# Kernel optimization log

Hardware: AMD Instinct MI355X
Metric: run time of the kernel (lower is better)

## Reference

```python
import jax, jax.numpy as jnp
import numpy as np

NUM_HEADS = 16


def setup_inputs() -> dict:
    key = jax.random.key(0)
    k1, k2, k3 = jax.random.split(key, 3)
    B, S, D = 4, 2048, 1024
    x = jax.random.normal(k1, (B, S, D), dtype=jnp.float32)
    w_qkv = jax.random.normal(k2, (D, 3 * D), dtype=jnp.float32) * 0.02
    b_qkv = jnp.zeros((3 * D,), dtype=jnp.float32)
    w_proj = jax.random.normal(k3, (D, D), dtype=jnp.float32) * 0.02
    b_proj = jnp.zeros((D,), dtype=jnp.float32)
    return {"x": x, "w_qkv": w_qkv, "b_qkv": b_qkv, "w_proj": w_proj, "b_proj": b_proj}


def reference(x, w_qkv, b_qkv, w_proj, b_proj):
    B, S, D = x.shape
    H = NUM_HEADS
    hd = D // H
    # fused qkv projection: [B,S,3D] -> [B,S,3H,hd]
    qkv = (x @ w_qkv + b_qkv).reshape(B, S, 3 * H, hd)
    q, k, v = jnp.split(qkv, 3, axis=2)  # each [B,S,H,hd]
    scale = (1.0 / jnp.sqrt(hd)).astype(x.dtype)
    scores = jnp.einsum("bqhd,bkhd->bhqk", q, k) * scale  # [B,H,S,S]
    causal = jnp.tril(jnp.ones((S, S), dtype=bool))  # [S,S]
    masked = jnp.where(causal, scores, jnp.finfo(scores.dtype).min)
    # softmax in fp32 reduce dtype, cast back (dropout_rate=0 -> identity)
    attn = jax.nn.softmax(masked.astype(jnp.float32)).astype(masked.dtype)
    out = jnp.einsum("bhqk,bkhd->bqhd", attn, v).reshape(B, S, D)
    return out @ w_proj + b_proj
```

## Files before the change

kernel.cpp:

```cpp
#include <hip/hip_runtime.h>
#include <hip/hip_bf16.h>

typedef __attribute__((ext_vector_type(8))) short short8;
typedef __attribute__((ext_vector_type(4))) float f32x4;

#define B_   4
#define S_   2048
#define D_   1024
#define H_   16
#define HD_  64
#define M_   (B_ * S_)
#define N3_  (3 * D_)

#define GLDS16(g, l)                                                        \
  __builtin_amdgcn_global_load_lds(                                         \
      (const __attribute__((address_space(1))) void*)(g),                   \
      (__attribute__((address_space(3))) void*)(l), 16, 0, 0)

template <int CTRL>
__device__ __forceinline__ float dpp_maxf(float x) {
  int v = __builtin_amdgcn_update_dpp(0, __builtin_bit_cast(int, x), CTRL,
                                      0xf, 0xf, true);
  return fmaxf(x, __builtin_bit_cast(float, v));
}
__device__ __forceinline__ float red16_max(float x) {
  x = dpp_maxf<0xB1>(x);
  x = dpp_maxf<0x4E>(x);
  x = dpp_maxf<0x141>(x);
  x = dpp_maxf<0x140>(x);
  return x;
}

__global__ __launch_bounds__(256) void cast_f32_bf16(
    const float* __restrict__ in, __hip_bfloat16* __restrict__ out, int n) {
  int i = (blockIdx.x * 256 + threadIdx.x) * 4;
  if (i + 3 < n) {
    float4 v = *(const float4*)(in + i);
    union { ushort4 u4; __hip_bfloat16 h[4]; } p;
    p.h[0] = __float2bfloat16(v.x);
    p.h[1] = __float2bfloat16(v.y);
    p.h[2] = __float2bfloat16(v.z);
    p.h[3] = __float2bfloat16(v.w);
    *(ushort4*)(out + i) = p.u4;
  }
}

__global__ __launch_bounds__(256) void transpose_cast(
    const float* __restrict__ in, __hip_bfloat16* __restrict__ out,
    int rows, int cols) {
  __shared__ float tile[32][33];
  int bx = blockIdx.x * 32;
  int by = blockIdx.y * 32;
  int tx = threadIdx.x, ty = threadIdx.y;
#pragma unroll
  for (int i = 0; i < 4; ++i)
    tile[ty + i * 8][tx] = in[(size_t)(by + ty + i * 8) * cols + bx + tx];
  __syncthreads();
#pragma unroll
  for (int i = 0; i < 4; ++i)
    out[(size_t)(bx + ty + i * 8) * rows + by + tx] =
        __float2bfloat16(tile[tx][ty + i * 8]);
}

__global__ __launch_bounds__(512) void transpose_v(
    const __hip_bfloat16* __restrict__ qkv, __hip_bfloat16* __restrict__ vt) {
  __shared__ __hip_bfloat16 tile[64][65];
  const int sb = blockIdx.x * 64;
  const int bh = blockIdx.y;
  const int b = bh >> 4, hh = bh & 15;
  const int tx = threadIdx.x, ty = threadIdx.y;
  const size_t src = (size_t)b * S_ * N3_ + 2 * D_ + hh * HD_;
#pragma unroll
  for (int i = 0; i < 8; ++i)
    tile[ty + i * 8][tx] = qkv[src + (size_t)(sb + ty + i * 8) * N3_ + tx];
  __syncthreads();
  const size_t dst = (size_t)bh * HD_ * S_;
#pragma unroll
  for (int i = 0; i < 8; ++i)
    vt[dst + (size_t)(ty + i * 8) * S_ + sb + tx] = tile[tx][ty + i * 8];
}

__device__ inline void store_out(float* p, float v) { *p = v; }
__device__ inline void store_out(__hip_bfloat16* p, float v) {
  *p = __float2bfloat16(v);
}

template <typename OUT_T>
__global__ __launch_bounds__(256) void gemm_bt_bias(
    const __hip_bfloat16* __restrict__ A, const __hip_bfloat16* __restrict__ Bt,
    const float* __restrict__ bias, OUT_T* __restrict__ C,
    int M, int N, int K) {
  __shared__ __align__(16) __hip_bfloat16 Alds[128 * 32];
  __shared__ __align__(16) __hip_bfloat16 Blds[128 * 32];
  const int t = threadIdx.x;
  const int wave = t >> 6, lane = t & 63;
  const int quad = lane >> 4, l15 = lane & 15;
  const int wm = (wave >> 1) * 64, wn = (wave & 1) * 64;
  const int m0 = blockIdx.y * 128, n0 = blockIdx.x * 128;

  const int rsub = lane >> 2;
  const int swz = (rsub ^ (rsub >> 2)) & 3;
  const int gcol = 8 * ((lane & 3) ^ swz);
  const int c0 = wave * 2, c1 = c0 + 1;
  const __hip_bfloat16* gA0 = A + (size_t)(m0 + c0 * 16 + rsub) * K + gcol;
  const __hip_bfloat16* gA1 = A + (size_t)(m0 + c1 * 16 + rsub) * K + gcol;
  const __hip_bfloat16* gB0 = Bt + (size_t)(n0 + c0 * 16 + rsub) * K + gcol;
  const __hip_bfloat16* gB1 = Bt + (size_t)(n0 + c1 * 16 + rsub) * K + gcol;
  __hip_bfloat16* lA0 = Alds + c0 * 512;
  __hip_bfloat16* lA1 = Alds + c1 * 512;
  __hip_bfloat16* lB0 = Blds + c0 * 512;
  __hip_bfloat16* lB1 = Blds + c1 * 512;
  const int swr = (l15 ^ (l15 >> 2)) & 3;
  const int fcol = 8 * (quad ^ swr);

  f32x4 acc[4][4] = {};

  for (int k0 = 0; k0 < K; k0 += 32) {
    GLDS16(gA0 + k0, lA0);
    GLDS16(gA1 + k0, lA1);
    GLDS16(gB0 + k0, lB0);
    GLDS16(gB1 + k0, lB1);
    __syncthreads();
    short8 a[4], bfr[4];
#pragma unroll
    for (int mt = 0; mt < 4; ++mt)
      a[mt] = *(const short8*)(Alds + (wm + mt * 16 + l15) * 32 + fcol);
#pragma unroll
    for (int nt = 0; nt < 4; ++nt)
      bfr[nt] = *(const short8*)(Blds + (wn + nt * 16 + l15) * 32 + fcol);
#pragma unroll
    for (int mt = 0; mt < 4; ++mt)
#pragma unroll
      for (int nt = 0; nt < 4; ++nt)
        acc[mt][nt] = __builtin_amdgcn_mfma_f32_16x16x32_bf16(
            a[mt], bfr[nt], acc[mt][nt], 0, 0, 0);
    __syncthreads();
  }

#pragma unroll
  for (int mt = 0; mt < 4; ++mt)
#pragma unroll
    for (int nt = 0; nt < 4; ++nt) {
      int col = n0 + wn + nt * 16 + l15;
      float bv = bias[col];
#pragma unroll
      for (int r = 0; r < 4; ++r) {
        int row = m0 + wm + mt * 16 + quad * 4 + r;
        store_out(C + (size_t)row * N + col, acc[mt][nt][r] + bv);
      }
    }
}

__global__ __launch_bounds__(256) void attn_causal(
    const __hip_bfloat16* __restrict__ qkv,
    const __hip_bfloat16* __restrict__ vt,
    __hip_bfloat16* __restrict__ ctx) {
  __shared__ __align__(16) __hip_bfloat16 Klds[64][72];
  __shared__ __align__(16) __hip_bfloat16 Vlds[64][72];
  __shared__ __align__(16) __hip_bfloat16 Plds[4][16][68];

  const int t = threadIdx.x;
  const int wave = t >> 6, lane = t & 63;
  const int quad = lane >> 4, l15 = lane & 15;
  const int xb = blockIdx.x, h = blockIdx.y, b = blockIdx.z;

  const size_t qbase = (size_t)b * S_ * N3_ + h * HD_;
  const size_t kbase = qbase + D_;
  const size_t vtbase = (size_t)(b * H_ + h) * HD_ * S_;
  const float C2 = 0.18033688f;

  short8 ones;
#pragma unroll
  for (int j = 0; j < 8; ++j) ones[j] = (short)0x3F80;

  for (int sel = 0; sel < 2; ++sel) {
    const int qb = sel ? (31 - xb) : xb;
    const int qrow = qb * 64 + wave * 16 + l15;
    short8 qf0 = *(const short8*)(qkv + qbase + (size_t)qrow * N3_ + quad * 8);
    short8 qf1 =
        *(const short8*)(qkv + qbase + (size_t)qrow * N3_ + 32 + quad * 8);

    f32x4 o[4] = {};
    float m_r[4], l_r[4];
#pragma unroll
    for (int r = 0; r < 4; ++r) { m_r[r] = -1e30f; l_r[r] = 0.f; }

    for (int kb = 0; kb <= qb; ++kb) {
#pragma unroll
      for (int i = 0; i < 2; ++i) {
        int c = t + 256 * i;
        int row = c >> 3, seg = c & 7;
        *(uint4*)(&Klds[row][seg * 8]) = *(const uint4*)(
            qkv + kbase + (size_t)(kb * 64 + row) * N3_ + seg * 8);
        *(uint4*)(&Vlds[row][seg * 8]) = *(const uint4*)(
            vt + vtbase + (size_t)row * S_ + kb * 64 + seg * 8);
      }
      __syncthreads();

      f32x4 s[4];
#pragma unroll
      for (int nt = 0; nt < 4; ++nt) {
        f32x4 z = {};
        short8 k0 = *(const short8*)(&Klds[nt * 16 + l15][quad * 8]);
        short8 k1 = *(const short8*)(&Klds[nt * 16 + l15][32 + quad * 8]);
        z = __builtin_amdgcn_mfma_f32_16x16x32_bf16(qf0, k0, z, 0, 0, 0);
        z = __builtin_amdgcn_mfma_f32_16x16x32_bf16(qf1, k1, z, 0, 0, 0);
        s[nt] = z;
      }
      const bool diag = (kb == qb);
#pragma unroll
      for (int nt = 0; nt < 4; ++nt)
#pragma unroll
        for (int r = 0; r < 4; ++r) {
          float v = s[nt][r] * C2;
          if (diag) {
            int colg = nt * 16 + l15;
            int rowg = wave * 16 + quad * 4 + r;
            if (colg > rowg) v = -1e30f;
          }
          s[nt][r] = v;
        }

      float alpha[4];
#pragma unroll
      for (int r = 0; r < 4; ++r) {
        float tm = fmaxf(fmaxf(s[0][r], s[1][r]), fmaxf(s[2][r], s[3][r]));
        tm = red16_max(tm);
        float mn = fmaxf(m_r[r], tm);
        alpha[r] = __builtin_amdgcn_exp2f(m_r[r] - mn);
        m_r[r] = mn;
      }

#pragma unroll
      for (int nt = 0; nt < 4; ++nt)
#pragma unroll
        for (int r = 0; r < 4; ++r) {
          float p = __builtin_amdgcn_exp2f(s[nt][r] - m_r[r]);
          Plds[wave][quad * 4 + r][nt * 16 + l15] = __float2bfloat16(p);
        }

#pragma unroll
      for (int dt = 0; dt < 4; ++dt)
#pragma unroll
        for (int r = 0; r < 4; ++r) o[dt][r] *= alpha[r];

      short8 p0 = *(const short8*)(&Plds[wave][l15][quad * 8]);
      short8 p1 = *(const short8*)(&Plds[wave][l15][32 + quad * 8]);
      f32x4 ps = {};
      ps = __builtin_amdgcn_mfma_f32_16x16x32_bf16(p0, ones, ps, 0, 0, 0);
      ps = __builtin_amdgcn_mfma_f32_16x16x32_bf16(p1, ones, ps, 0, 0, 0);
#pragma unroll
      for (int r = 0; r < 4; ++r) l_r[r] = alpha[r] * l_r[r] + ps[r];

#pragma unroll
      for (int dt = 0; dt < 4; ++dt) {
        short8 v0 = *(const short8*)(&Vlds[dt * 16 + l15][quad * 8]);
        short8 v1 = *(const short8*)(&Vlds[dt * 16 + l15][32 + quad * 8]);
        o[dt] = __builtin_amdgcn_mfma_f32_16x16x32_bf16(p0, v0, o[dt], 0, 0, 0);
        o[dt] = __builtin_amdgcn_mfma_f32_16x16x32_bf16(p1, v1, o[dt], 0, 0, 0);
      }
      __syncthreads();
    }

#pragma unroll
    for (int dt = 0; dt < 4; ++dt)
#pragma unroll
      for (int r = 0; r < 4; ++r) {
        int rowg = qb * 64 + wave * 16 + quad * 4 + r;
        ctx[((size_t)b * S_ + rowg) * D_ + h * HD_ + dt * 16 + l15] =
            __float2bfloat16(o[dt][r] / l_r[r]);
      }
  }
}

extern "C" void kernel_launch(void* const* d_in, const int* in_sizes, int n_in,
                              void* d_out, int out_size, void* d_ws,
                              size_t ws_size, hipStream_t stream) {
  const float* x      = (const float*)d_in[0];
  const float* w_qkv  = (const float*)d_in[1];
  const float* b_qkv  = (const float*)d_in[2];
  const float* w_proj = (const float*)d_in[3];
  const float* b_proj = (const float*)d_in[4];
  float* out = (float*)d_out;

  char* ws = (char*)d_ws;
  __hip_bfloat16* xb     = (__hip_bfloat16*)(ws + 0);
  __hip_bfloat16* vtb    = (__hip_bfloat16*)(ws + 0);
  __hip_bfloat16* wqkvT  = (__hip_bfloat16*)(ws + 16777216);
  __hip_bfloat16* wprojT = (__hip_bfloat16*)(ws + 23068672);
  __hip_bfloat16* qkvb   = (__hip_bfloat16*)(ws + 25165824);
  __hip_bfloat16* ctx    = (__hip_bfloat16*)(ws + 75497472);

  cast_f32_bf16<<<8192, 256, 0, stream>>>(x, xb, M_ * D_);
  transpose_cast<<<dim3(N3_ / 32, D_ / 32), dim3(32, 8), 0, stream>>>(
      w_qkv, wqkvT, D_, N3_);
  transpose_cast<<<dim3(D_ / 32, D_ / 32), dim3(32, 8), 0, stream>>>(
      w_proj, wprojT, D_, D_);

  gemm_bt_bias<__hip_bfloat16><<<dim3(N3_ / 128, M_ / 128), 256, 0, stream>>>(
      xb, wqkvT, b_qkv, qkvb, M_, N3_, D_);

  transpose_v<<<dim3(S_ / 64, B_ * H_), dim3(64, 8), 0, stream>>>(qkvb, vtb);

  attn_causal<<<dim3(16, H_, B_), 256, 0, stream>>>(qkvb, vtb, ctx);

  gemm_bt_bias<float><<<dim3(D_ / 128, M_ / 128), 256, 0, stream>>>(
      ctx, wprojT, b_proj, out, M_, D_, D_);
}
```

Baseline: 308.7 us.

## Fuse V transpose into QKV GEMM, widen K tile, transpose attention MFMA layout

The QKV GEMM now writes the V columns straight into the transposed per-head layout, so the separate transpose_v kernel and its extra pass over memory go away. Both GEMMs use a 64-wide K tile with an XOR swizzle, which halves the barrier count per K step. The attention kernel swaps MFMA operand order so each lane holds one query row. That turns the row max into two shuffles, the scale into an FMA, P stores into packed vector writes, and the output normalisation into a reciprocal with packed stores. It costs more LDS per GEMM block, which may lower occupancy, and the V writes are strided 8-byte stores.

New measurement: 289.6 us. -6.2%, faster.

```diff
diff --git a/kernel.cpp b/kernel.cpp
--- a/kernel.cpp
+++ b/kernel.cpp
@@ -17,18 +17,11 @@
       (const __attribute__((address_space(1))) void*)(g),                   \
       (__attribute__((address_space(3))) void*)(l), 16, 0, 0)
 
-template <int CTRL>
-__device__ __forceinline__ float dpp_maxf(float x) {
-  int v = __builtin_amdgcn_update_dpp(0, __builtin_bit_cast(int, x), CTRL,
-                                      0xf, 0xf, true);
-  return fmaxf(x, __builtin_bit_cast(float, v));
-}
-__device__ __forceinline__ float red16_max(float x) {
-  x = dpp_maxf<0xB1>(x);
-  x = dpp_maxf<0x4E>(x);
-  x = dpp_maxf<0x141>(x);
-  x = dpp_maxf<0x140>(x);
-  return x;
+__device__ __forceinline__ unsigned pack_bf2(float a, float b) {
+  union { __hip_bfloat16 h; unsigned short s; } ua, ub;
+  ua.h = __float2bfloat16(a);
+  ub.h = __float2bfloat16(b);
+  return (unsigned)ua.s | ((unsigned)ub.s << 16);
 }
 
 __global__ __launch_bounds__(256) void cast_f32_bf16(
@@ -62,93 +55,98 @@
         __float2bfloat16(tile[tx][ty + i * 8]);
 }
 
-__global__ __launch_bounds__(512) void transpose_v(
-    const __hip_bfloat16* __restrict__ qkv, __hip_bfloat16* __restrict__ vt) {
-  __shared__ __hip_bfloat16 tile[64][65];
-  const int sb = blockIdx.x * 64;
-  const int bh = blockIdx.y;
-  const int b = bh >> 4, hh = bh & 15;
-  const int tx = threadIdx.x, ty = threadIdx.y;
-  const size_t src = (size_t)b * S_ * N3_ + 2 * D_ + hh * HD_;
-#pragma unroll
-  for (int i = 0; i < 8; ++i)
-    tile[ty + i * 8][tx] = qkv[src + (size_t)(sb + ty + i * 8) * N3_ + tx];
-  __syncthreads();
-  const size_t dst = (size_t)bh * HD_ * S_;
-#pragma unroll
-  for (int i = 0; i < 8; ++i)
-    vt[dst + (size_t)(ty + i * 8) * S_ + sb + tx] = tile[tx][ty + i * 8];
-}
-
 __device__ inline void store_out(float* p, float v) { *p = v; }
 __device__ inline void store_out(__hip_bfloat16* p, float v) {
   *p = __float2bfloat16(v);
 }
 
-template <typename OUT_T>
+template <typename OUT_T, bool WVT>
 __global__ __launch_bounds__(256) void gemm_bt_bias(
     const __hip_bfloat16* __restrict__ A, const __hip_bfloat16* __restrict__ Bt,
     const float* __restrict__ bias, OUT_T* __restrict__ C,
-    int M, int N, int K) {
-  __shared__ __align__(16) __hip_bfloat16 Alds[128 * 32];
-  __shared__ __align__(16) __hip_bfloat16 Blds[128 * 32];
+    __hip_bfloat16* __restrict__ vt, int M, int N, int K) {
+  __shared__ __align__(16) __hip_bfloat16 Alds[128 * 64];
+  __shared__ __align__(16) __hip_bfloat16 Blds[128 * 64];
   const int t = threadIdx.x;
   const int wave = t >> 6, lane = t & 63;
   const int quad = lane >> 4, l15 = lane & 15;
   const int wm = (wave >> 1) * 64, wn = (wave & 1) * 64;
   const int m0 = blockIdx.y * 128, n0 = blockIdx.x * 128;
 
-  const int rsub = lane >> 2;
-  const int swz = (rsub ^ (rsub >> 2)) & 3;
-  const int gcol = 8 * ((lane & 3) ^ swz);
-  const int c0 = wave * 2, c1 = c0 + 1;
-  const __hip_bfloat16* gA0 = A + (size_t)(m0 + c0 * 16 + rsub) * K + gcol;
-  const __hip_bfloat16* gA1 = A + (size_t)(m0 + c1 * 16 + rsub) * K + gcol;
-  const __hip_bfloat16* gB0 = Bt + (size_t)(n0 + c0 * 16 + rsub) * K + gcol;
-  const __hip_bfloat16* gB1 = Bt + (size_t)(n0 + c1 * 16 + rsub) * K + gcol;
-  __hip_bfloat16* lA0 = Alds + c0 * 512;
-  __hip_bfloat16* lA1 = Alds + c1 * 512;
-  __hip_bfloat16* lB0 = Blds + c0 * 512;
-  __hip_bfloat16* lB1 = Blds + c1 * 512;
-  const int swr = (l15 ^ (l15 >> 2)) & 3;
-  const int fcol = 8 * (quad ^ swr);
+  const int rsub = lane >> 3;
+  const int gc16 = (lane & 7) ^ (rsub & 7);
+  const __hip_bfloat16* gA[4];
+  const __hip_bfloat16* gB[4];
+  __hip_bfloat16* lA[4];
+  __hip_bfloat16* lB[4];
+#pragma unroll
+  for (int i = 0; i < 4; ++i) {
+    int c = wave * 4 + i;
+    int row = c * 8 + rsub;
+    gA[i] = A + (size_t)(m0 + row) * K + gc16 * 8;
+    gB[i] = Bt + (size_t)(n0 + row) * K + gc16 * 8;
+    lA[i] = Alds + c * 512;
+    lB[i] = Blds + c * 512;
+  }
 
   f32x4 acc[4][4] = {};
 
-  for (int k0 = 0; k0 < K; k0 += 32) {
-    GLDS16(gA0 + k0, lA0);
-    GLDS16(gA1 + k0, lA1);
-    GLDS16(gB0 + k0, lB0);
-    GLDS16(gB1 + k0, lB1);
+  for (int k0 = 0; k0 < K; k0 += 64) {
+#pragma unroll
+    for (int i = 0; i < 4; ++i) {
+      GLDS16(gA[i] + k0, lA[i]);
+      GLDS16(gB[i] + k0, lB[i]);
+    }
     __syncthreads();
-    short8 a[4], bfr[4];
+#pragma unroll
+    for (int kk = 0; kk < 2; ++kk) {
+      const int fo = ((kk * 4 + quad) ^ (l15 & 7)) * 8;
+      short8 a[4], bfr[4];
+#pragma unroll
+      for (int mt = 0; mt < 4; ++mt)
+        a[mt] = *(const short8*)(Alds + (wm + mt * 16 + l15) * 64 + fo);
+#pragma unroll
+      for (int nt = 0; nt < 4; ++nt)
+        bfr[nt] = *(const short8*)(Blds + (wn + nt * 16 + l15) * 64 + fo);
+#pragma unroll
+      for (int mt = 0; mt < 4; ++mt)
+#pragma unroll
+        for (int nt = 0; nt < 4; ++nt)
+          acc[mt][nt] = __builtin_amdgcn_mfma_f32_16x16x32_bf16(
+              a[mt], bfr[nt], acc[mt][nt], 0, 0, 0);
+    }
+    __syncthreads();
+  }
+
+  if (WVT && n0 >= 2048) {
 #pragma unroll
     for (int mt = 0; mt < 4; ++mt)
-      a[mt] = *(const short8*)(Alds + (wm + mt * 16 + l15) * 32 + fcol);
-#pragma unroll
-    for (int nt = 0; nt < 4; ++nt)
-      bfr[nt] = *(const short8*)(Blds + (wn + nt * 16 + l15) * 32 + fcol);
+#pragma unroll
+      for (int nt = 0; nt < 4; ++nt) {
+        int col = n0 + wn + nt * 16 + l15;
+        float bv = bias[col];
+        int hv = (col - 2048) >> 6, d = (col - 2048) & 63;
+        int row0 = m0 + wm + mt * 16 + quad * 4;
+        int bidx = row0 >> 11, s = row0 & 2047;
+        uint2 w;
+        w.x = pack_bf2(acc[mt][nt][0] + bv, acc[mt][nt][1] + bv);
+        w.y = pack_bf2(acc[mt][nt][2] + bv, acc[mt][nt][3] + bv);
+        *(uint2*)(vt + ((size_t)(bidx * 16 + hv) * 64 + d) * 2048 + s) = w;
+      }
+  } else {
 #pragma unroll
     for (int mt = 0; mt < 4; ++mt)
 #pragma unroll
-      for (int nt = 0; nt < 4; ++nt)
-        acc[mt][nt] = __builtin_amdgcn_mfma_f32_16x16x32_bf16(
-            a[mt], bfr[nt], acc[mt][nt], 0, 0, 0);
-    __syncthreads();
-  }
-
-#pragma unroll
-  for (int mt = 0; mt < 4; ++mt)
-#pragma unroll
-    for (int nt = 0; nt < 4; ++nt) {
-      int col = n0 + wn + nt * 16 + l15;
-      float bv = bias[col];
-#pragma unroll
-      for (int r = 0; r < 4; ++r) {
-        int row = m0 + wm + mt * 16 + quad * 4 + r;
-        store_out(C + (size_t)row * N + col, acc[mt][nt][r] + bv);
-      }
-    }
+      for (int nt = 0; nt < 4; ++nt) {
+        int col = n0 + wn + nt * 16 + l15;
+        float bv = bias[col];
+#pragma unroll
+        for (int r = 0; r < 4; ++r) {
+          int row = m0 + wm + mt * 16 + quad * 4 + r;
+          store_out(C + (size_t)row * N + col, acc[mt][nt][r] + bv);
+        }
+      }
+  }
 }
 
 __global__ __launch_bounds__(256) void attn_causal(
@@ -157,7 +155,7 @@
     __hip_bfloat16* __restrict__ ctx) {
   __shared__ __align__(16) __hip_bfloat16 Klds[64][72];
   __shared__ __align__(16) __hip_bfloat16 Vlds[64][72];
-  __shared__ __align__(16) __hip_bfloat16 Plds[4][16][68];
+  __shared__ __align__(16) __hip_bfloat16 Plds[4][16][72];
 
   const int t = threadIdx.x;
   const int wave = t >> 6, lane = t & 63;
@@ -181,9 +179,7 @@
         *(const short8*)(qkv + qbase + (size_t)qrow * N3_ + 32 + quad * 8);
 
     f32x4 o[4] = {};
-    float m_r[4], l_r[4];
-#pragma unroll
-    for (int r = 0; r < 4; ++r) { m_r[r] = -1e30f; l_r[r] = 0.f; }
+    float m_r = -1e30f, l_r = 0.f;
 
     for (int kb = 0; kb <= qb; ++kb) {
 #pragma unroll
@@ -197,79 +193,80 @@
       }
       __syncthreads();
 
-      f32x4 s[4];
+      f32x4 st[4];
 #pragma unroll
       for (int nt = 0; nt < 4; ++nt) {
         f32x4 z = {};
         short8 k0 = *(const short8*)(&Klds[nt * 16 + l15][quad * 8]);
         short8 k1 = *(const short8*)(&Klds[nt * 16 + l15][32 + quad * 8]);
-        z = __builtin_amdgcn_mfma_f32_16x16x32_bf16(qf0, k0, z, 0, 0, 0);
-        z = __builtin_amdgcn_mfma_f32_16x16x32_bf16(qf1, k1, z, 0, 0, 0);
-        s[nt] = z;
-      }
-      const bool diag = (kb == qb);
+        z = __builtin_amdgcn_mfma_f32_16x16x32_bf16(k0, qf0, z, 0, 0, 0);
+        z = __builtin_amdgcn_mfma_f32_16x16x32_bf16(k1, qf1, z, 0, 0, 0);
+        st[nt] = z;
+      }
+      if (kb == qb) {
+        const int rloc = wave * 16 + l15;
+#pragma unroll
+        for (int nt = 0; nt < 4; ++nt)
+#pragma unroll
+          for (int r = 0; r < 4; ++r)
+            if (nt * 16 + quad * 4 + r > rloc) st[nt][r] = -1e30f;
+      }
+
+      float tm = st[0][0];
 #pragma unroll
       for (int nt = 0; nt < 4; ++nt)
 #pragma unroll
-        for (int r = 0; r < 4; ++r) {
-          float v = s[nt][r] * C2;
-          if (diag) {
-            int colg = nt * 16 + l15;
-            int rowg = wave * 16 + quad * 4 + r;
-            if (colg > rowg) v = -1e30f;
-          }
-          s[nt][r] = v;
-        }
-
-      float alpha[4];
-#pragma unroll
-      for (int r = 0; r < 4; ++r) {
-        float tm = fmaxf(fmaxf(s[0][r], s[1][r]), fmaxf(s[2][r], s[3][r]));
-        tm = red16_max(tm);
-        float mn = fmaxf(m_r[r], tm);
-        alpha[r] = __builtin_amdgcn_exp2f(m_r[r] - mn);
-        m_r[r] = mn;
-      }
-
-#pragma unroll
-      for (int nt = 0; nt < 4; ++nt)
-#pragma unroll
-        for (int r = 0; r < 4; ++r) {
-          float p = __builtin_amdgcn_exp2f(s[nt][r] - m_r[r]);
-          Plds[wave][quad * 4 + r][nt * 16 + l15] = __float2bfloat16(p);
-        }
+        for (int r = 0; r < 4; ++r) tm = fmaxf(tm, st[nt][r]);
+      tm = fmaxf(tm, __shfl_xor(tm, 16));
+      tm = fmaxf(tm, __shfl_xor(tm, 32));
+      const float mn = fmaxf(m_r, tm * C2);
+      const float alpha = __builtin_amdgcn_exp2f(m_r - mn);
+      m_r = mn;
+
+#pragma unroll
+      for (int nt = 0; nt < 4; ++nt) {
+        float p0 = __builtin_amdgcn_exp2f(__builtin_fmaf(st[nt][0], C2, -mn));
+        float p1 = __builtin_amdgcn_exp2f(__builtin_fmaf(st[nt][1], C2, -mn));
+        float p2 = __builtin_amdgcn_exp2f(__builtin_fmaf(st[nt][2], C2, -mn));
+        float p3 = __builtin_amdgcn_exp2f(__builtin_fmaf(st[nt][3], C2, -mn));
+        uint2 w;
+        w.x = pack_bf2(p0, p1);
+        w.y = pack_bf2(p2, p3);
+        *(uint2*)(&Plds[wave][l15][nt * 16 + quad * 4]) = w;
+      }
 
 #pragma unroll
       for (int dt = 0; dt < 4; ++dt)
 #pragma unroll
-        for (int r = 0; r < 4; ++r) o[dt][r] *= alpha[r];
-
-      short8 p0 = *(const short8*)(&Plds[wave][l15][quad * 8]);
-      short8 p1 = *(const short8*)(&Plds[wave][l15][32 + quad * 8]);
+        for (int r = 0; r < 4; ++r) o[dt][r] *= alpha;
+
+      short8 pB0 = *(const short8*)(&Plds[wave][l15][quad * 8]);
+      short8 pB1 = *(const short8*)(&Plds[wave][l15][32 + quad * 8]);
+
       f32x4 ps = {};
-      ps = __builtin_amdgcn_mfma_f32_16x16x32_bf16(p0, ones, ps, 0, 0, 0);
-      ps = __builtin_amdgcn_mfma_f32_16x16x32_bf16(p1, ones, ps, 0, 0, 0);
-#pragma unroll
-      for (int r = 0; r < 4; ++r) l_r[r] = alpha[r] * l_r[r] + ps[r];
+      ps = __builtin_amdgcn_mfma_f32_16x16x32_bf16(ones, pB0, ps, 0, 0, 0);
+      ps = __builtin_amdgcn_mfma_f32_16x16x32_bf16(ones, pB1, ps, 0, 0, 0);
+      l_r = alpha * l_r + ps[0];
 
 #pragma unroll
       for (int dt = 0; dt < 4; ++dt) {
         short8 v0 = *(const short8*)(&Vlds[dt * 16 + l15][quad * 8]);
         short8 v1 = *(const short8*)(&Vlds[dt * 16 + l15][32 + quad * 8]);
-        o[dt] = __builtin_amdgcn_mfma_f32_16x16x32_bf16(p0, v0, o[dt], 0, 0, 0);
-        o[dt] = __builtin_amdgcn_mfma_f32_16x16x32_bf16(p1, v1, o[dt], 0, 0, 0);
+        o[dt] = __builtin_amdgcn_mfma_f32_16x16x32_bf16(v0, pB0, o[dt], 0, 0, 0);
+        o[dt] = __builtin_amdgcn_mfma_f32_16x16x32_bf16(v1, pB1, o[dt], 0, 0, 0);
       }
       __syncthreads();
     }
 
-#pragma unroll
-    for (int dt = 0; dt < 4; ++dt)
-#pragma unroll
-      for (int r = 0; r < 4; ++r) {
-        int rowg = qb * 64 + wave * 16 + quad * 4 + r;
-        ctx[((size_t)b * S_ + rowg) * D_ + h * HD_ + dt * 16 + l15] =
-            __float2bfloat16(o[dt][r] / l_r[r]);
-      }
+    const float rl = __builtin_amdgcn_rcpf(l_r);
+    __hip_bfloat16* crow = ctx + ((size_t)b * S_ + qrow) * D_ + h * HD_;
+#pragma unroll
+    for (int dt = 0; dt < 4; ++dt) {
+      uint2 w;
+      w.x = pack_bf2(o[dt][0] * rl, o[dt][1] * rl);
+      w.y = pack_bf2(o[dt][2] * rl, o[dt][3] * rl);
+      *(uint2*)(crow + dt * 16 + quad * 4) = w;
+    }
   }
 }
 
@@ -290,6 +287,7 @@
   __hip_bfloat16* wprojT = (__hip_bfloat16*)(ws + 23068672);
   __hip_bfloat16* qkvb   = (__hip_bfloat16*)(ws + 25165824);
   __hip_bfloat16* ctx    = (__hip_bfloat16*)(ws + 75497472);
+  __hip_bfloat16* vt2    = (__hip_bfloat16*)(ws + 91750400);
 
   cast_f32_bf16<<<8192, 256, 0, stream>>>(x, xb, M_ * D_);
   transpose_cast<<<dim3(N3_ / 32, D_ / 32), dim3(32, 8), 0, stream>>>(
@@ -297,13 +295,12 @@
   transpose_cast<<<dim3(D_ / 32, D_ / 32), dim3(32, 8), 0, stream>>>(
       w_proj, wprojT, D_, D_);
 
-  gemm_bt_bias<__hip_bfloat16><<<dim3(N3_ / 128, M_ / 128), 256, 0, stream>>>(
-      xb, wqkvT, b_qkv, qkvb, M_, N3_, D_);
-
-  transpose_v<<<dim3(S_ / 64, B_ * H_), dim3(64, 8), 0, stream>>>(qkvb, vtb);
-
-  attn_causal<<<dim3(16, H_, B_), 256, 0, stream>>>(qkvb, vtb, ctx);
-
-  gemm_bt_bias<float><<<dim3(D_ / 128, M_ / 128), 256, 0, stream>>>(
-      ctx, wprojT, b_proj, out, M_, D_, D_);
-}
+  gemm_bt_bias<__hip_bfloat16, true>
+      <<<dim3(N3_ / 128, M_ / 128), 256, 0, stream>>>(
+          xb, wqkvT, b_qkv, qkvb, vt2, M_, N3_, D_);
+
+  attn_causal<<<dim3(16, H_, B_), 256, 0, stream>>>(qkvb, vt2, ctx);
+
+  gemm_bt_bias<float, false><<<dim3(D_ / 128, M_ / 128), 256, 0, stream>>>(
+      ctx, wprojT, b_proj, out, (__hip_bfloat16*)nullptr, M_, D_, D_);
+}
```
